# Kernel optimization log

Hardware: AMD Instinct MI355X
Metric: run time of the kernel (lower is better)

## Reference

```python
import jax, jax.numpy as jnp
import numpy as np

B, T, D, H = 64, 512, 512, 1024


def setup_inputs() -> dict:
    key = jax.random.key(0)
    k1, k2 = jax.random.split(key, 2)
    x = jax.random.normal(k1, (B, T, D), dtype=jnp.float32)
    W = jax.random.normal(k2, (D, H), dtype=jnp.float32) * 0.02
    b = jnp.zeros((H,), dtype=jnp.float32)
    return {"x": x, "W": W, "b": b}


def reference(x, W, b):
    # Step model (docstring example of RecurrentWrapper):
    #   h_new = sigmoid(h + relu(x_t @ W + b))
    # The Dense projection is time-independent, so hoist it out of the scan
    # (same math as applying it per step inside tf.scan).
    proj = jax.nn.relu(jnp.einsum('btd,dh->bth', x, W) + b)  # [B,T,H]
    proj_t = jnp.swapaxes(proj, 0, 1)  # [T,B,H], matches _swap_time_and_samples
    h0 = jnp.zeros((x.shape[0], W.shape[1]), dtype=x.dtype)  # zeros initial state

    def step(h, p_t):
        h_new = jax.nn.sigmoid(h + p_t)
        return h_new, h_new

    _, hs = jax.lax.scan(step, h0, proj_t)  # [T,B,H]
    return jnp.swapaxes(hs, 0, 1)  # [B,T,H] (return_sequences=True)
```

## Files before the change

### kernel.cpp

```cpp
#include <hip/hip_runtime.h>
#include <hip/hip_bf16.h>
#include <stdint.h>

#define B_ 64
#define T_ 512
#define D_ 512
#define H_ 1024
#define M_ (B_*T_)
#define K_ D_
#define N_ H_

#define BM 128
#define BNF 128
#define BK 64
#define NKT (K_/BK)

#define BN 128

typedef __attribute__((ext_vector_type(4))) float f32x4;
typedef __attribute__((ext_vector_type(8))) short s16x8;
typedef __attribute__((ext_vector_type(4))) short s16x4;
typedef unsigned short u16;

__device__ __forceinline__ short f2bf(float f) {
  __bf16 h = (__bf16)f;
  return __builtin_bit_cast(short, h);
}
__device__ __forceinline__ float bf2f(u16 u) {
  return __builtin_bit_cast(float, ((unsigned)u) << 16);
}
__device__ __forceinline__ s16x4 cvt4(f32x4 v) {
  s16x4 r;
  r[0] = f2bf(v[0]); r[1] = f2bf(v[1]);
  r[2] = f2bf(v[2]); r[3] = f2bf(v[3]);
  return r;
}
__device__ __forceinline__ void gload_lds16(const void* g, void* l) {
  __builtin_amdgcn_global_load_lds(
      (const __attribute__((address_space(1))) void*)g,
      (__attribute__((address_space(3))) void*)l, 16, 0, 0);
}


__global__ __launch_bounds__(256)
void prep(const float* __restrict__ x, const float* __restrict__ W,
          u16* __restrict__ xb, u16* __restrict__ wt) {
  __shared__ u16 Lt[64 * 72];
  const int tid = threadIdx.x;

  if (blockIdx.x < 128) {
    const int n0 = (blockIdx.x & 15) * 64;
    const int k0 = (blockIdx.x >> 4) * 64;
    #pragma unroll
    for (int p = 0; p < 16; ++p) {
      const int idx = p * 256 + tid;
      const int r = idx >> 6;
      const int c = idx & 63;
      const float v = W[(size_t)(k0 + r) * H_ + n0 + c];
      Lt[c * 72 + r] = (u16)f2bf(v);
    }
    __syncthreads();
    #pragma unroll
    for (int p = 0; p < 2; ++p) {
      const int idx = p * 256 + tid;
      const int rn = idx >> 3;
      const int ck = (idx & 7) * 8;
      const s16x8 v = *(const s16x8*)&Lt[rn * 72 + ck];
      *(s16x8*)&wt[(size_t)(n0 + rn) * K_ + k0 + ck] = v;
    }
  } else {
    const int nvec = M_ * K_ / 8;
    const int stride = 2048 * 256;
    for (int i = (blockIdx.x - 128) * 256 + tid; i < nvec; i += stride) {
      f32x4 a = ((const f32x4*)x)[2*i];
      f32x4 b = ((const f32x4*)x)[2*i + 1];
      s16x8 r;
      r[0]=f2bf(a[0]); r[1]=f2bf(a[1]); r[2]=f2bf(a[2]); r[3]=f2bf(a[3]);
      r[4]=f2bf(b[0]); r[5]=f2bf(b[1]); r[6]=f2bf(b[2]); r[7]=f2bf(b[3]);
      ((s16x8*)xb)[i] = r;
    }
  }
}

__global__ __launch_bounds__(256, 2)
void fused_gemm_scan(const u16* __restrict__ xb, const u16* __restrict__ wt,
                     const float* __restrict__ bias, float* __restrict__ out) {
  __shared__ char Asm[BM * BK * 2];
  __shared__ char Bsm[BNF * BK * 2];
  __shared__ char Pt[BM * BNF * 2];

  const int tid  = threadIdx.x;
  const int lane = tid & 63;
  const int wave = tid >> 6;

  const int rb  = blockIdx.x;
  const int xcd = rb & 7;
  const int idx = rb >> 3;
  const int b   = xcd * 8 + (idx & 7);
  const int ht  = idx >> 3;
  const int n0  = ht * BNF;

  const int g  = lane >> 4;
  const int lr = lane & 15;
  const int wr = wave >> 1;
  const int wc = wave & 1;
  const int rSub = lane >> 3;
  const int kec  = ((lane & 7) ^ rSub) * 8;

  float bv[4];
  #pragma unroll
  for (int n = 0; n < 4; ++n)
    bv[n] = bias[n0 + wc*64 + n*16 + lr];

  const int hcol = tid;
  float hh = 0.f;

  #pragma unroll 1
  for (int tc = 0; tc < 4; ++tc) {
    const int m0 = b * T_ + tc * BM;

    f32x4 acc[4][4];
    #pragma unroll
    for (int m = 0; m < 4; ++m)
      #pragma unroll
      for (int n = 0; n < 4; ++n)
        acc[m][n] = (f32x4){0.f, 0.f, 0.f, 0.f};

    #pragma unroll 1
    for (int kt = 0; kt < NKT; ++kt) {
      if (kt) __syncthreads();
      const int k0 = kt * BK;
      #pragma unroll
      for (int p = 0; p < 4; ++p) {
        const int slot = wave * 4 + p;
        const int r = slot * 8 + rSub;
        gload_lds16(xb + (size_t)(m0 + r) * K_ + k0 + kec, Asm + slot * 1024);
      }
      #pragma unroll
      for (int p = 0; p < 4; ++p) {
        const int slot = wave * 4 + p;
        const int r = slot * 8 + rSub;
        gload_lds16(wt + (size_t)(n0 + r) * K_ + k0 + kec, Bsm + slot * 1024);
      }
      __syncthreads();

      #pragma unroll
      for (int kk = 0; kk < BK; kk += 32) {
        s16x8 af[4], bf[4];
        #pragma unroll
        for (int m = 0; m < 4; ++m) {
          const int row = wr*64 + m*16 + lr;
          af[m] = *(const s16x8*)(Asm + row*128 +
                                  ((kk*2 + g*16) ^ ((row & 7) << 4)));
        }
        #pragma unroll
        for (int n = 0; n < 4; ++n) {
          const int row = wc*64 + n*16 + lr;
          bf[n] = *(const s16x8*)(Bsm + row*128 +
                                  ((kk*2 + g*16) ^ ((row & 7) << 4)));
        }
        #pragma unroll
        for (int m = 0; m < 4; ++m)
          #pragma unroll
          for (int n = 0; n < 4; ++n)
            acc[m][n] = __builtin_amdgcn_mfma_f32_16x16x32_bf16(
                af[m], bf[n], acc[m][n], 0, 0, 0);
      }
    }

    #pragma unroll
    for (int m = 0; m < 4; ++m) {
      #pragma unroll
      for (int n = 0; n < 4; ++n) {
        const int col2 = (wc*64 + n*16 + lr) * 2;
        #pragma unroll
        for (int j = 0; j < 4; ++j) {
          const int row = wr*64 + m*16 + g*4 + j;
          *(u16*)(Pt + row*256 + (col2 ^ (((row>>2)&7) << 5))) =
              (u16)f2bf(fmaxf(acc[m][n][j] + bv[n], 0.f));
        }
      }
    }
    __syncthreads();

    if (tid < 128) {
      float* o = out + (size_t)(b * T_ + tc * BM) * H_ + n0 + hcol;
      const int c2 = hcol * 2;
      #pragma unroll 8
      for (int t = 0; t < BM; ++t) {
        const float v = bf2f(*(const u16*)(Pt + t*256 + (c2 ^ (((t>>2)&7) << 5))));
        hh = __builtin_amdgcn_rcpf(1.f + __expf(-(hh + v)));
        o[(size_t)t * H_] = hh;
      }
    }
    __syncthreads();
  }
}


__global__ __launch_bounds__(256, 2)
void gemm_bias_relu(const float* __restrict__ X, const float* __restrict__ W,
                    const float* __restrict__ bias, float* __restrict__ out) {
  __shared__ char Asm[BM*BK*2];
  __shared__ char Bsm[BN*BK*2];

  const int tid  = threadIdx.x;
  const int lane = tid & 63;
  const int wave = tid >> 6;
  const int m0 = blockIdx.x * BM;
  const int n0 = blockIdx.y * BN;

  const int arow  = tid >> 4;
  const int acol4 = (tid & 15) << 2;
  const int brow  = tid >> 5;
  const int bn4   = (tid & 31) << 2;

  const int g  = lane >> 4;
  const int lr = lane & 15;
  const int wr = wave >> 1;
  const int wc = wave & 1;

  s16x4 aRegs[8], bRegs[8];
  f32x4 acc[4][4];
  #pragma unroll
  for (int m = 0; m < 4; ++m)
    #pragma unroll
    for (int n = 0; n < 4; ++n)
      acc[m][n] = (f32x4){0.f, 0.f, 0.f, 0.f};

  auto loadTile = [&](int kt) {
    const int k0 = kt * BK;
    #pragma unroll
    for (int p = 0; p < 8; ++p) {
      const int r = p*16 + arow;
      f32x4 av = *(const f32x4*)(X + (size_t)(m0 + r)*K_ + k0 + acol4);
      aRegs[p] = cvt4(av);
      const int kk = p*8 + brow;
      f32x4 bv = *(const f32x4*)(W + (size_t)(k0 + kk)*N_ + n0 + bn4);
      bRegs[p] = cvt4(bv);
    }
  };
  auto writeTile = [&]() {
    #pragma unroll
    for (int p = 0; p < 8; ++p) {
      const int r = p*16 + arow;
      const int ao = ((r*BK + acol4) * 2) ^ ((r & 7) << 4);
      *(s16x4*)(Asm + ao) = aRegs[p];
      const int kk = p*8 + brow;
      #pragma unroll
      for (int i = 0; i < 4; ++i) {
        const int n = bn4 + i;
        const int bo = ((n*BK + kk) * 2) ^ ((n & 7) << 4);
        *(short*)(Bsm + bo) = bRegs[p][i];
      }
    }
  };
  auto mfmaTile = [&]() {
    #pragma unroll
    for (int kk = 0; kk < BK; kk += 32) {
      s16x8 af[4], bf[4];
      #pragma unroll
      for (int m = 0; m < 4; ++m) {
        const int r = wr*64 + m*16 + lr;
        af[m] = *(const s16x8*)(Asm + (((r*BK + kk + g*8) * 2) ^ ((r & 7) << 4)));
      }
      #pragma unroll
      for (int n = 0; n < 4; ++n) {
        const int c = wc*64 + n*16 + lr;
        bf[n] = *(const s16x8*)(Bsm + (((c*BK + kk + g*8) * 2) ^ ((c & 7) << 4)));
      }
      #pragma unroll
      for (int m = 0; m < 4; ++m)
        #pragma unroll
        for (int n = 0; n < 4; ++n)
          acc[m][n] = __builtin_amdgcn_mfma_f32_16x16x32_bf16(
              af[m], bf[n], acc[m][n], 0, 0, 0);
    }
  };

  loadTile(0);
  #pragma unroll 1
  for (int kt = 0; kt < NKT; ++kt) {
    if (kt) __syncthreads();
    writeTile();
    __syncthreads();
    if (kt + 1 < NKT) loadTile(kt + 1);
    mfmaTile();
  }

  float bv[4];
  #pragma unroll
  for (int n = 0; n < 4; ++n)
    bv[n] = bias[n0 + wc*64 + n*16 + lr];
  #pragma unroll
  for (int m = 0; m < 4; ++m)
    #pragma unroll
    for (int n = 0; n < 4; ++n) {
      const int col = n0 + wc*64 + n*16 + lr;
      #pragma unroll
      for (int j = 0; j < 4; ++j) {
        const int row = m0 + wr*64 + m*16 + g*4 + j;
        out[(size_t)row*N_ + col] = fmaxf(acc[m][n][j] + bv[n], 0.f);
      }
    }
}

#define PF 16
__global__ __launch_bounds__(256)
void scan_sigmoid(float* __restrict__ out) {
  const int tid = blockIdx.x * blockDim.x + threadIdx.x;
  const int b = tid >> 10;
  const int h = tid & (H_ - 1);
  float* p = out + (size_t)b * (T_ * H_) + h;

  float buf[PF];
  #pragma unroll
  for (int i = 0; i < PF; ++i) buf[i] = p[(size_t)i * H_];

  float hh = 0.f;
  #pragma unroll 1
  for (int t0 = 0; t0 < T_ - PF; t0 += PF) {
    #pragma unroll
    for (int i = 0; i < PF; ++i) {
      const float v = buf[i];
      buf[i] = p[(size_t)(t0 + i + PF) * H_];
      hh = __builtin_amdgcn_rcpf(1.f + __expf(-(hh + v)));
      p[(size_t)(t0 + i) * H_] = hh;
    }
  }
  #pragma unroll
  for (int i = 0; i < PF; ++i) {
    const float v = buf[i];
    hh = __builtin_amdgcn_rcpf(1.f + __expf(-(hh + v)));
    p[(size_t)(T_ - PF + i) * H_] = hh;
  }
}


extern "C" void kernel_launch(void* const* d_in, const int* in_sizes, int n_in,
                              void* d_out, int out_size, void* d_ws, size_t ws_size,
                              hipStream_t stream) {
  const float* x    = (const float*)d_in[0];
  const float* W    = (const float*)d_in[1];
  const float* bias = (const float*)d_in[2];
  float* out = (float*)d_out;

  const size_t XB = (size_t)M_ * K_ * 2;
  const size_t WT = (size_t)N_ * K_ * 2;

  if (ws_size >= XB + WT) {
    u16* xb = (u16*)d_ws;
    u16* wt = (u16*)((char*)d_ws + XB);

    prep<<<2176, 256, 0, stream>>>(x, W, xb, wt);
    fused_gemm_scan<<<B_ * (N_/BNF), 256, 0, stream>>>(xb, wt, bias, out);
  } else {
    gemm_bias_relu<<<dim3(M_/BM, N_/BN), 256, 0, stream>>>(x, W, bias, out);
    scan_sigmoid<<<(B_*H_)/256, 256, 0, stream>>>(out);
  }
}
```

Measured before the change: 84.51 us.

## Double-buffer GEMM K-tiles in LDS with prefetch of next tile

Replaces the single-buffered BK=64 LDS staging with two BK=32 buffers. The next K-slice is loaded asynchronously via global_load_lds while MFMAs run on the current one, which should hide global-load latency behind compute. A new packed, swizzled LDS layout (two rows per 128-byte line) keeps reads conflict-free. The cost is twice as many barriers per K, and it relies on the async LDS loads completing before the barrier.

```diff
diff --git a/kernel.cpp b/kernel.cpp
--- a/kernel.cpp
+++ b/kernel.cpp
@@ -12,10 +12,11 @@
 
 #define BM 128
 #define BNF 128
+#define BKP 32
+#define NPH (K_/BKP)
+#define BN 128
 #define BK 64
 #define NKT (K_/BK)
-
-#define BN 128
 
 typedef __attribute__((ext_vector_type(4))) float f32x4;
 typedef __attribute__((ext_vector_type(8))) short s16x8;
@@ -39,6 +40,12 @@
   __builtin_amdgcn_global_load_lds(
       (const __attribute__((address_space(1))) void*)g,
       (__attribute__((address_space(3))) void*)l, 16, 0, 0);
+}
+
+__device__ __forceinline__ int packoff(int row, int g) {
+  const int j = row >> 1;
+  const int s = (((row & 1) * 4 + g) ^ (j & 7));
+  return j * 128 + s * 16;
 }
 
 
@@ -85,8 +92,8 @@
 __global__ __launch_bounds__(256, 2)
 void fused_gemm_scan(const u16* __restrict__ xb, const u16* __restrict__ wt,
                      const float* __restrict__ bias, float* __restrict__ out) {
-  __shared__ char Asm[BM * BK * 2];
-  __shared__ char Bsm[BNF * BK * 2];
+  __shared__ char Ab[2 * BM * BKP * 2];
+  __shared__ char Bb[2 * BNF * BKP * 2];
   __shared__ char Pt[BM * BNF * 2];
 
   const int tid  = threadIdx.x;
@@ -104,8 +111,6 @@
   const int lr = lane & 15;
   const int wr = wave >> 1;
   const int wc = wave & 1;
-  const int rSub = lane >> 3;
-  const int kec  = ((lane & 7) ^ rSub) * 8;
 
   float bv[4];
   #pragma unroll
@@ -114,6 +119,21 @@
 
   const int hcol = tid;
   float hh = 0.f;
+
+  auto stage2 = [&](char* Ad, char* Bd, int m0_, int k0) {
+    #pragma unroll
+    for (int l = 0; l < 2; ++l) {
+      const int f = l * 256 + tid;
+      const int j = f >> 3, s = f & 7;
+      const int sp = s ^ (j & 7);
+      const int row = 2*j + (sp >> 2);
+      const int kc8 = (sp & 3) * 8;
+      char* dA = Ad + l * 4096 + wave * 1024;
+      char* dB = Bd + l * 4096 + wave * 1024;
+      gload_lds16(xb + (size_t)(m0_ + row) * K_ + k0 + kc8, dA);
+      gload_lds16(wt + (size_t)(n0  + row) * K_ + k0 + kc8, dB);
+    }
+  };
 
   #pragma unroll 1
   for (int tc = 0; tc < 4; ++tc) {
@@ -126,46 +146,35 @@
       for (int n = 0; n < 4; ++n)
         acc[m][n] = (f32x4){0.f, 0.f, 0.f, 0.f};
 
+    stage2(Ab, Bb, m0, 0);
+    __syncthreads();
+
+    char* Ac = Ab;        char* Bc = Bb;
+    char* An = Ab + 8192; char* Bn = Bb + 8192;
+
     #pragma unroll 1
-    for (int kt = 0; kt < NKT; ++kt) {
-      if (kt) __syncthreads();
-      const int k0 = kt * BK;
-      #pragma unroll
-      for (int p = 0; p < 4; ++p) {
-        const int slot = wave * 4 + p;
-        const int r = slot * 8 + rSub;
-        gload_lds16(xb + (size_t)(m0 + r) * K_ + k0 + kec, Asm + slot * 1024);
-      }
-      #pragma unroll
-      for (int p = 0; p < 4; ++p) {
-        const int slot = wave * 4 + p;
-        const int r = slot * 8 + rSub;
-        gload_lds16(wt + (size_t)(n0 + r) * K_ + k0 + kec, Bsm + slot * 1024);
-      }
+    for (int ph = 0; ph < NPH; ++ph) {
+      if (ph + 1 < NPH)
+        stage2(An, Bn, m0, (ph + 1) * BKP);
+
+      s16x8 af[4], bf[4];
+      #pragma unroll
+      for (int m = 0; m < 4; ++m)
+        af[m] = *(const s16x8*)(Ac + packoff(wr*64 + m*16 + lr, g));
+      #pragma unroll
+      for (int n = 0; n < 4; ++n)
+        bf[n] = *(const s16x8*)(Bc + packoff(wc*64 + n*16 + lr, g));
+      #pragma unroll
+      for (int m = 0; m < 4; ++m)
+        #pragma unroll
+        for (int n = 0; n < 4; ++n)
+          acc[m][n] = __builtin_amdgcn_mfma_f32_16x16x32_bf16(
+              af[m], bf[n], acc[m][n], 0, 0, 0);
+
       __syncthreads();
-
-      #pragma unroll
-      for (int kk = 0; kk < BK; kk += 32) {
-        s16x8 af[4], bf[4];
-        #pragma unroll
-        for (int m = 0; m < 4; ++m) {
-          const int row = wr*64 + m*16 + lr;
-          af[m] = *(const s16x8*)(Asm + row*128 +
-                                  ((kk*2 + g*16) ^ ((row & 7) << 4)));
-        }
-        #pragma unroll
-        for (int n = 0; n < 4; ++n) {
-          const int row = wc*64 + n*16 + lr;
-          bf[n] = *(const s16x8*)(Bsm + row*128 +
-                                  ((kk*2 + g*16) ^ ((row & 7) << 4)));
-        }
-        #pragma unroll
-        for (int m = 0; m < 4; ++m)
-          #pragma unroll
-          for (int n = 0; n < 4; ++n)
-            acc[m][n] = __builtin_amdgcn_mfma_f32_16x16x32_bf16(
-                af[m], bf[n], acc[m][n], 0, 0, 0);
-      }
+      char* t;
+      t = Ac; Ac = An; An = t;
+      t = Bc; Bc = Bn; Bn = t;
     }
 
     #pragma unroll
```

New measurement: 87.73 us. 3.8% more time.

## Fuse fp32-to-bf16 conversion of x into GEMM A-tile staging with register prefetch

Applied to the files above, without the earlier changes.

The separate pass that converted all of x to bf16 in a workspace is removed. The GEMM now loads fp32 x tiles into registers one k-step ahead, converts them, and writes swizzled bf16 into LDS, while W still goes through a small prep kernel and direct-to-LDS loads. This saves one full write and read of the bf16 copy of x (about 32 MB of traffic) and one kernel's worth of work. In exchange, each GEMM block reads fp32 x, which is twice the bytes. Every x tile is also re-read by the 8 column blocks, which relies on L2 hits, and the prefetch uses more registers.

```diff
diff --git a/kernel.cpp b/kernel.cpp
--- a/kernel.cpp
+++ b/kernel.cpp
@@ -43,47 +43,32 @@
 
 
 __global__ __launch_bounds__(256)
-void prep(const float* __restrict__ x, const float* __restrict__ W,
-          u16* __restrict__ xb, u16* __restrict__ wt) {
+void prep_w(const float* __restrict__ W, u16* __restrict__ wt) {
   __shared__ u16 Lt[64 * 72];
+  const int n0 = ((int)blockIdx.x & 15) * 64;
+  const int k0 = ((int)blockIdx.x >> 4) * 64;
   const int tid = threadIdx.x;
-
-  if (blockIdx.x < 128) {
-    const int n0 = (blockIdx.x & 15) * 64;
-    const int k0 = (blockIdx.x >> 4) * 64;
-    #pragma unroll
-    for (int p = 0; p < 16; ++p) {
-      const int idx = p * 256 + tid;
-      const int r = idx >> 6;
-      const int c = idx & 63;
-      const float v = W[(size_t)(k0 + r) * H_ + n0 + c];
-      Lt[c * 72 + r] = (u16)f2bf(v);
-    }
-    __syncthreads();
-    #pragma unroll
-    for (int p = 0; p < 2; ++p) {
-      const int idx = p * 256 + tid;
-      const int rn = idx >> 3;
-      const int ck = (idx & 7) * 8;
-      const s16x8 v = *(const s16x8*)&Lt[rn * 72 + ck];
-      *(s16x8*)&wt[(size_t)(n0 + rn) * K_ + k0 + ck] = v;
-    }
-  } else {
-    const int nvec = M_ * K_ / 8;
-    const int stride = 2048 * 256;
-    for (int i = (blockIdx.x - 128) * 256 + tid; i < nvec; i += stride) {
-      f32x4 a = ((const f32x4*)x)[2*i];
-      f32x4 b = ((const f32x4*)x)[2*i + 1];
-      s16x8 r;
-      r[0]=f2bf(a[0]); r[1]=f2bf(a[1]); r[2]=f2bf(a[2]); r[3]=f2bf(a[3]);
-      r[4]=f2bf(b[0]); r[5]=f2bf(b[1]); r[6]=f2bf(b[2]); r[7]=f2bf(b[3]);
-      ((s16x8*)xb)[i] = r;
-    }
+  #pragma unroll
+  for (int p = 0; p < 16; ++p) {
+    const int idx = p * 256 + tid;
+    const int r = idx >> 6;
+    const int c = idx & 63;
+    const float v = W[(size_t)(k0 + r) * H_ + n0 + c];
+    Lt[c * 72 + r] = (u16)f2bf(v);
+  }
+  __syncthreads();
+  #pragma unroll
+  for (int p = 0; p < 2; ++p) {
+    const int idx = p * 256 + tid;
+    const int rn = idx >> 3;
+    const int ck = (idx & 7) * 8;
+    const s16x8 v = *(const s16x8*)&Lt[rn * 72 + ck];
+    *(s16x8*)&wt[(size_t)(n0 + rn) * K_ + k0 + ck] = v;
   }
 }
 
 __global__ __launch_bounds__(256, 2)
-void fused_gemm_scan(const u16* __restrict__ xb, const u16* __restrict__ wt,
+void fused_gemm_scan(const float* __restrict__ X, const u16* __restrict__ wt,
                      const float* __restrict__ bias, float* __restrict__ out) {
   __shared__ char Asm[BM * BK * 2];
   __shared__ char Bsm[BNF * BK * 2];
@@ -107,6 +92,9 @@
   const int rSub = lane >> 3;
   const int kec  = ((lane & 7) ^ rSub) * 8;
 
+  const int arow = tid >> 3;
+  const int ac   = tid & 7;
+
   float bv[4];
   #pragma unroll
   for (int n = 0; n < 4; ++n)
@@ -114,6 +102,37 @@
 
   const int hcol = tid;
   float hh = 0.f;
+
+  f32x4 pre[8];
+
+  auto loadA = [&](int m0_, int k0) {
+    #pragma unroll
+    for (int p = 0; p < 4; ++p) {
+      const float* s = X + (size_t)(m0_ + p*32 + arow) * K_ + k0 + ac*8;
+      pre[2*p]   = *(const f32x4*)s;
+      pre[2*p+1] = *(const f32x4*)(s + 4);
+    }
+  };
+  auto writeA = [&]() {
+    #pragma unroll
+    for (int p = 0; p < 4; ++p) {
+      const int row = p*32 + arow;
+      s16x8 r;
+      r[0]=f2bf(pre[2*p][0]);   r[1]=f2bf(pre[2*p][1]);
+      r[2]=f2bf(pre[2*p][2]);   r[3]=f2bf(pre[2*p][3]);
+      r[4]=f2bf(pre[2*p+1][0]); r[5]=f2bf(pre[2*p+1][1]);
+      r[6]=f2bf(pre[2*p+1][2]); r[7]=f2bf(pre[2*p+1][3]);
+      *(s16x8*)(Asm + row*128 + ((ac*16) ^ ((row & 7) << 4))) = r;
+    }
+  };
+  auto stageB = [&](int k0) {
+    #pragma unroll
+    for (int p = 0; p < 4; ++p) {
+      const int slot = wave * 4 + p;
+      const int r = slot * 8 + rSub;
+      gload_lds16(wt + (size_t)(n0 + r) * K_ + k0 + kec, Bsm + slot * 1024);
+    }
+  };
 
   #pragma unroll 1
   for (int tc = 0; tc < 4; ++tc) {
@@ -126,22 +145,15 @@
       for (int n = 0; n < 4; ++n)
         acc[m][n] = (f32x4){0.f, 0.f, 0.f, 0.f};
 
+    loadA(m0, 0);
+
     #pragma unroll 1
     for (int kt = 0; kt < NKT; ++kt) {
       if (kt) __syncthreads();
-      const int k0 = kt * BK;
-      #pragma unroll
-      for (int p = 0; p < 4; ++p) {
-        const int slot = wave * 4 + p;
-        const int r = slot * 8 + rSub;
-        gload_lds16(xb + (size_t)(m0 + r) * K_ + k0 + kec, Asm + slot * 1024);
-      }
-      #pragma unroll
-      for (int p = 0; p < 4; ++p) {
-        const int slot = wave * 4 + p;
-        const int r = slot * 8 + rSub;
-        gload_lds16(wt + (size_t)(n0 + r) * K_ + k0 + kec, Bsm + slot * 1024);
-      }
+      stageB(kt * BK);
+      writeA();
+      if (kt + 1 < NKT)
+        loadA(m0, (kt + 1) * BK);
       __syncthreads();
 
       #pragma unroll
@@ -345,15 +357,12 @@
   const float* bias = (const float*)d_in[2];
   float* out = (float*)d_out;
 
-  const size_t XB = (size_t)M_ * K_ * 2;
   const size_t WT = (size_t)N_ * K_ * 2;
 
-  if (ws_size >= XB + WT) {
-    u16* xb = (u16*)d_ws;
-    u16* wt = (u16*)((char*)d_ws + XB);
-
-    prep<<<2176, 256, 0, stream>>>(x, W, xb, wt);
-    fused_gemm_scan<<<B_ * (N_/BNF), 256, 0, stream>>>(xb, wt, bias, out);
+  if (ws_size >= WT) {
+    u16* wt = (u16*)d_ws;
+    prep_w<<<128, 256, 0, stream>>>(W, wt);
+    fused_gemm_scan<<<B_ * (N_/BNF), 256, 0, stream>>>(x, wt, bias, out);
   } else {
     gemm_bias_relu<<<dim3(M_/BM, N_/BN), 256, 0, stream>>>(x, W, bias, out);
     scan_sigmoid<<<(B_*H_)/256, 256, 0, stream>>>(out);
```

Measured after the change: 81.58 us. 1.04x faster.
